# Kernel tuning notes

Measured on AMD Instinct MI355X. Metric: run time of the kernel, lower is better.

Reference implementation:

```python
import jax, jax.numpy as jnp
import numpy as np

DIM = 512
HEADS = 4
MARGIN = 1.0


def _attn_pool(x, Wq, bq, Wk, bk, Wv, bv, Wo, bo):
    # SelfAttention(video_dim, m_dim=DIM, heads=HEADS) followed by mean over time
    B, T, _ = x.shape
    hd = DIM // HEADS
    q = (x @ Wq + bq).reshape(B, T, HEADS, hd)
    k = (x @ Wk + bk).reshape(B, T, HEADS, hd)
    v = (x @ Wv + bv).reshape(B, T, HEADS, hd)
    a = jax.nn.softmax(jnp.einsum('bthd,bshd->bhts', q, k) / jnp.sqrt(jnp.float32(hd)), axis=-1)
    out = jnp.einsum('bhts,bshd->bthd', a, v).reshape(B, T, DIM) @ Wo + bo
    return out.mean(axis=1)  # [B, DIM]


def _ranking(x1, x2, gmask, margin):
    # vectorized form of the per-row torch.roll loop:
    # s[i, b] = <x1[b], x2[(b - i) mod B]>
    B = x1.shape[0]
    idx = (jnp.arange(B)[None, :] - jnp.arange(B)[:, None]) % B  # [B, B]
    s = jnp.einsum('bc,ibc->ib', x1, x2[idx])                    # [B, B]
    mask = gmask[idx] & gmask[None, :]                           # [B, B]
    # max-margin ranking loss with per-column masked mean, then mean over valid cols
    loss = jnp.maximum(0.0, margin + s[1:] - s[0:1])             # [B-1, B]
    m = mask[1:]
    cnt = m.sum(axis=0)
    col_mean = jnp.where(cnt > 0, (loss * m).sum(axis=0) / jnp.maximum(cnt, 1), 0.0)
    valid = cnt > 0
    loss_val = jnp.sum(col_mean * valid) / jnp.maximum(valid.sum(), 1)
    # ranking accuracy: idx==0 iff the true (row 0) score is max among selected
    sel_sum = jnp.sum(jnp.where(mask, s, 0.0), axis=0)
    col_valid = (sel_sum != 0) & mask.any(axis=0)
    s_masked = jnp.where(mask, s, -jnp.inf)
    top_is_first = (s[0] >= s_masked.max(axis=0)).astype(jnp.float32)
    acc = jnp.sum(jnp.where(col_valid, top_is_first, 0.0)) / jnp.maximum(col_valid.sum(), 1)
    return loss_val, jax.lax.stop_gradient(acc)


def setup_inputs() -> dict:
    key = jax.random.key(0)
    ks = iter(jax.random.split(key, 64))

    def nrm(shape, s=0.02):
        return jax.random.normal(next(ks), shape, jnp.float32) * s

    inp = {
        'o': jax.random.normal(next(ks), (128, 1024, DIM), jnp.float32),
        'rgb': jax.random.normal(next(ks), (128, 64, 2048), jnp.float32),
        'audio': jax.random.normal(next(ks), (128, 64, 128), jnp.float32),
        'group_mask': jax.random.randint(next(ks), (128,), 0, 2).astype(bool),
    }
    for name, d in (('rgb', 2048), ('audio', 128)):
        inp[f'{name}_Wq'] = nrm((d, DIM)); inp[f'{name}_bq'] = jnp.zeros((DIM,), jnp.float32)
        inp[f'{name}_Wk'] = nrm((d, DIM)); inp[f'{name}_bk'] = jnp.zeros((DIM,), jnp.float32)
        inp[f'{name}_Wv'] = nrm((d, DIM)); inp[f'{name}_bv'] = jnp.zeros((DIM,), jnp.float32)
        inp[f'{name}_Wo'] = nrm((DIM, DIM)); inp[f'{name}_bo'] = jnp.zeros((DIM,), jnp.float32)
        inp[f'{name}_W2'] = nrm((DIM, DIM)); inp[f'{name}_b2'] = jnp.zeros((DIM,), jnp.float32)
    inp['expand_W'] = nrm((DIM, 2 * DIM))
    inp['expand_b'] = jnp.zeros((2 * DIM,), jnp.float32)
    return inp


def reference(o, rgb, audio, group_mask,
              rgb_Wq, rgb_bq, rgb_Wk, rgb_bk, rgb_Wv, rgb_bv, rgb_Wo, rgb_bo, rgb_W2, rgb_b2,
              audio_Wq, audio_bq, audio_Wk, audio_bk, audio_Wv, audio_bv, audio_Wo, audio_bo,
              audio_W2, audio_b2, expand_W, expand_b):
    # per-modality encoders (CollaborativeGating multiplies are discarded in the
    # original forward, so gating is a no-op on the output -> skipped)
    f_rgb = _attn_pool(rgb, rgb_Wq, rgb_bq, rgb_Wk, rgb_bk, rgb_Wv, rgb_bv, rgb_Wo, rgb_bo) @ rgb_W2 + rgb_b2
    f_aud = _attn_pool(audio, audio_Wq, audio_bq, audio_Wk, audio_bk, audio_Wv, audio_bv, audio_Wo, audio_bo) @ audio_W2 + audio_b2
    feat = jnp.concatenate([f_rgb, f_aud], axis=-1)  # [B, 2*DIM]
    oo = o.mean(axis=-2) @ expand_W + expand_b       # [B, 2*DIM]
    oo = oo / jnp.maximum(jnp.linalg.norm(oo, axis=-1, keepdims=True), 1e-12)
    l1, a1 = _ranking(oo, feat, group_mask, MARGIN)
    l2, a2 = _ranking(feat, oo, group_mask, MARGIN)
    loss = l1 + l2
    acc = (a1 + a2) / 2.0
    return loss, acc
```

## Files before the change

kernel.cpp:

```cpp
#include <hip/hip_runtime.h>
#include <hip/hip_bf16.h>
#include <math.h>


using bf16x8 = __attribute__((ext_vector_type(8))) __bf16;
using f32x4  = __attribute__((ext_vector_type(4))) float;

enum : size_t {
  B_PART = 0,
  B_OM   = B_PART + (size_t)128*16*2*512*4,
  B_OO   = B_OM   + (size_t)128*512*4,
  B_G    = B_OO   + (size_t)128*1024*4,
  B_PP   = B_G    + (size_t)128*128*4,
  B_PO   = B_PP   + (size_t)2*128*512*4,
  B_FEAT = B_PO   + (size_t)2*128*512*4,
  B_QBF  = B_FEAT + (size_t)2*128*512*4,
  B_KBF  = B_QBF  + (size_t)2*8192*512*2,
  B_VBF  = B_KBF  + (size_t)2*8192*512*2,
  B_XR   = B_VBF  + (size_t)2*8192*512*2,
  B_XA   = B_XR   + (size_t)8192*2048*2,
  B_WT   = B_XA   + (size_t)8192*128*2,
  B_END  = B_WT   + (size_t)3*512*2048*2 + (size_t)3*512*128*2
};

__device__ __forceinline__ unsigned short f2bf(float f) {
  __hip_bfloat16 h = __float2bfloat16(f);
  return __builtin_bit_cast(unsigned short, h);
}
__device__ __forceinline__ unsigned pack2(float a, float b) {
  return (unsigned)f2bf(a) | ((unsigned)f2bf(b) << 16);
}

struct PrepArgs {
  const float* xr; unsigned short* xrb;
  const float* xa; unsigned short* xab;
  const float* w[6];
  unsigned short* wt[6];
};

__device__ __forceinline__ void castT64(const float* __restrict__ W,
                                        unsigned short* __restrict__ Wt,
                                        int K, int n0, int k0, int tid) {
  __shared__ float t[64][65];
  int c = tid & 63, r4 = tid >> 6;
#pragma unroll
  for (int i = 0; i < 16; ++i) {
    int r = r4 * 16 + i;
    t[c][r] = W[(size_t)(k0 + r) * 512 + n0 + c];
  }
  __syncthreads();
  int nr = tid >> 3, kk = (tid & 7) * 8;
#pragma unroll
  for (int p = 0; p < 2; ++p) {
    int n = nr + p * 32;
    float4 x0 = *(const float4*)&t[n][kk];
    float4 x1 = *(const float4*)&t[n][kk + 4];
    uint4 pk;
    pk.x = pack2(x0.x, x0.y); pk.y = pack2(x0.z, x0.w);
    pk.z = pack2(x1.x, x1.y); pk.w = pack2(x1.z, x1.w);
    *(uint4*)&Wt[(size_t)(n0 + n) * K + k0 + kk] = pk;
  }
}

__device__ __forceinline__ void cast8(const float* __restrict__ x,
                                      unsigned short* __restrict__ y,
                                      int i, int stride, int total) {
  for (; i < total; i += stride) {
    float4 v0 = *(const float4*)(x + (size_t)i * 8);
    float4 v1 = *(const float4*)(x + (size_t)i * 8 + 4);
    uint4 pk;
    pk.x = pack2(v0.x, v0.y); pk.y = pack2(v0.z, v0.w);
    pk.z = pack2(v1.x, v1.y); pk.w = pack2(v1.z, v1.w);
    *(uint4*)(y + (size_t)i * 8) = pk;
  }
}

__global__ __launch_bounds__(256) void prep_k(PrepArgs a) {
  int bid = blockIdx.x, tid = threadIdx.x;
  if (bid < 768) {
    int w = bid >> 8, t = bid & 255;
    castT64(a.w[w], a.wt[w], 2048, (t >> 5) * 64, (t & 31) * 64, tid);
  } else if (bid < 816) {
    int t = bid - 768; int w = t >> 4; t &= 15;
    castT64(a.w[3 + w], a.wt[3 + w], 128, (t >> 1) * 64, (t & 1) * 64, tid);
  } else if (bid < 1840) {
    cast8(a.xr, a.xrb, (bid - 816) * 256 + tid, 262144, 2097152);
  } else {
    cast8(a.xa, a.xab, (bid - 1840) * 256 + tid, 16384, 131072);
  }
}

struct QkvAll {
  const unsigned short* A[2];
  const unsigned short* Wt[6];
  const float* bias[6];
  unsigned short* out[6];
  const float* o; float* part;
};

__device__ __forceinline__ void stage16(const void* g, void* l) {
  __builtin_amdgcn_global_load_lds((const __attribute__((address_space(1))) void*)g,
                                   (__attribute__((address_space(3))) void*)l, 16, 0, 0);
}

__global__ __launch_bounds__(256) void qkv_mean_k(QkvAll args) {
  __shared__ __align__(16) char smem[32768];

  int id = blockIdx.x;
  int blk = id / 448, off = id % 448;

  if (off >= 192) {
    int mb = blk * 256 + (off - 192);
    int c = mb & 15, b = mb >> 4;
    const float* base = args.o + ((size_t)b * 1024 + (size_t)c * 64) * 512;
    int tid = threadIdx.x;
    int d4 = (tid & 127) << 2, half = tid >> 7;
    float4 s = {0.f, 0.f, 0.f, 0.f};
    for (int t = half; t < 64; t += 2) {
      float4 v = *(const float4*)(base + (size_t)t * 512 + d4);
      s.x += v.x; s.y += v.y; s.z += v.z; s.w += v.w;
    }
    *(float4*)(args.part + (((size_t)b * 16 + c) * 2 + half) * 512 + d4) = s;
    return;
  }

  int qid = blk * 192 + off;
  int mi = qid >= 768 ? 1 : 0; qid -= mi * 768;
  int by = qid & 63, bx = (qid >> 6) & 3, bz = qid >> 8;
  int K = mi ? 128 : 2048;
  int nt = K >> 5;
  const unsigned short* A = args.A[mi];
  int wi = mi * 3 + bz;
  const unsigned short* Bt = args.Wt[wi];
  const float* bias = args.bias[wi];

  int tid = threadIdx.x;
  int l = tid & 63, w = tid >> 6;
  int row0 = by * 128, col0 = bx * 128;
  int wrow = (w & 1) * 64, wcol = (w >> 1) * 64;
  int kg = l >> 4, lr = l & 15;

  float bv[4];
#pragma unroll
  for (int n = 0; n < 4; ++n) bv[n] = bias[col0 + wcol + n * 16 + lr];
  asm volatile("" :: "v"(bv[0]), "v"(bv[1]), "v"(bv[2]), "v"(bv[3]));

  auto stage_pair = [&](char* dbuf, int k0s) {
#pragma unroll
    for (int i = 0; i < 2; ++i) {
      int c = w * 128 + i * 64 + l;
      int B_ = c << 4;
      int e6 = ((B_ >> 6) ^ (B_ >> 8)) & 1;
      int E  = B_ ^ (e6 << 4) ^ (((B_ >> 7) & 1) << 5) ^ (((B_ >> 8) & 1) << 6);
      int r = E >> 6, s = ((E >> 4) & 3) << 3;
      stage16(A + (size_t)(row0 + r) * K + k0s + s, dbuf + (w * 128 + i * 64) * 16);
      stage16(Bt + (size_t)(col0 + r) * K + k0s + s, dbuf + 8192 + (w * 128 + i * 64) * 16);
    }
  };

  f32x4 acc[4][4] = {};
  int xorA = (lr & 7) << 4;

  stage_pair(smem, 0);
  int cur = 0;
  for (int t = 0; t < nt; ++t) {
    if (t + 1 < nt) {
      stage_pair(smem + ((cur ^ 1) << 14), (t + 1) << 5);
      asm volatile("s_waitcnt vmcnt(4)" ::: "memory");
    } else {
      asm volatile("s_waitcnt vmcnt(0)" ::: "memory");
    }
    __builtin_amdgcn_s_barrier();
    __builtin_amdgcn_sched_barrier(0);

    const char* Ab = smem + (cur << 14);
    const char* Bb = Ab + 8192;
    bf16x8 af[4], bfr[4];
#pragma unroll
    for (int m = 0; m < 4; ++m) {
      int ra = wrow + m * 16 + lr;
      int rb = wcol + m * 16 + lr;
      af[m]  = *(const bf16x8*)(Ab + (((ra << 6) + (kg << 4)) ^ xorA));
      bfr[m] = *(const bf16x8*)(Bb + (((rb << 6) + (kg << 4)) ^ xorA));
    }
#pragma unroll
    for (int m = 0; m < 4; ++m)
#pragma unroll
      for (int n = 0; n < 4; ++n)
        acc[m][n] = __builtin_amdgcn_mfma_f32_16x16x32_bf16(af[m], bfr[n], acc[m][n], 0, 0, 0);

    __builtin_amdgcn_sched_barrier(0);
    __builtin_amdgcn_s_barrier();
    cur ^= 1;
  }

  float* cst = (float*)(smem) + w * 1024;
  unsigned short* C = args.out[wi];
  int rr = l >> 3, q = l & 7;
#pragma unroll
  for (int m = 0; m < 4; ++m) {
#pragma unroll
    for (int n = 0; n < 4; ++n) {
      int g0 = (n * 16 + lr) >> 3, o0 = lr & 7;
#pragma unroll
      for (int j = 0; j < 4; ++j) {
        int row = kg * 4 + j;
        cst[row * 64 + (((g0 ^ (row & 7)) << 3) | o0)] = acc[m][n][j] + bv[n];
      }
    }
#pragma unroll
    for (int p = 0; p < 2; ++p) {
      int row = rr + p * 8;
      int grp = q ^ (row & 7);
      float4 x0 = *(const float4*)&cst[row * 64 + grp * 8];
      float4 x1 = *(const float4*)&cst[row * 64 + grp * 8 + 4];
      uint4 pk;
      pk.x = pack2(x0.x, x0.y); pk.y = pack2(x0.z, x0.w);
      pk.z = pack2(x1.x, x1.y); pk.w = pack2(x1.z, x1.w);
      *(uint4*)&C[(size_t)(row0 + wrow + m * 16 + row) * 512 + col0 + wcol + q * 8] = pk;
    }
  }
}

__global__ __launch_bounds__(512) void finalize_mean_k(const float* __restrict__ part,
                                                       float* __restrict__ om) {
  int b = blockIdx.x, d = threadIdx.x;
  float s = 0.f;
  for (int c = 0; c < 32; ++c) s += part[((size_t)b * 32 + c) * 512 + d];
  om[(size_t)b * 512 + d] = s * (1.f / 1024.f);
}

__global__ __launch_bounds__(256) void gemm_f32_k(
    const float* __restrict__ A, int lda,
    const float* __restrict__ W, int ldw,
    const float* __restrict__ bias,
    float* __restrict__ C, int ldc, int K) {
  __shared__ float As[16][65];
  __shared__ float Ws[16][64];
  int tid = threadIdx.x;
  int tx = tid & 15, ty = tid >> 4;
  int row0 = blockIdx.y * 64, col0 = blockIdx.x * 64;
  float acc[4][4] = {};
  int ar = tid >> 2, ac = (tid & 3) << 2;
  int wr = tid >> 4, wc = (tid & 15) << 2;
  for (int k0 = 0; k0 < K; k0 += 16) {
    float4 av = *(const float4*)(A + (size_t)(row0 + ar) * lda + k0 + ac);
    As[ac + 0][ar] = av.x; As[ac + 1][ar] = av.y;
    As[ac + 2][ar] = av.z; As[ac + 3][ar] = av.w;
    float4 wv = *(const float4*)(W + (size_t)(k0 + wr) * ldw + col0 + wc);
    *(float4*)&Ws[wr][wc] = wv;
    __syncthreads();
#pragma unroll
    for (int k = 0; k < 16; ++k) {
      float a0 = As[k][(ty << 2) + 0], a1 = As[k][(ty << 2) + 1];
      float a2 = As[k][(ty << 2) + 2], a3 = As[k][(ty << 2) + 3];
      float4 w = *(const float4*)&Ws[k][tx << 2];
      acc[0][0] += a0 * w.x; acc[0][1] += a0 * w.y; acc[0][2] += a0 * w.z; acc[0][3] += a0 * w.w;
      acc[1][0] += a1 * w.x; acc[1][1] += a1 * w.y; acc[1][2] += a1 * w.z; acc[1][3] += a1 * w.w;
      acc[2][0] += a2 * w.x; acc[2][1] += a2 * w.y; acc[2][2] += a2 * w.z; acc[2][3] += a2 * w.w;
      acc[3][0] += a3 * w.x; acc[3][1] += a3 * w.y; acc[3][2] += a3 * w.z; acc[3][3] += a3 * w.w;
    }
    __syncthreads();
  }
  float4 bv = *(const float4*)(bias + col0 + (tx << 2));
#pragma unroll
  for (int i = 0; i < 4; ++i) {
    float4 ov;
    ov.x = acc[i][0] + bv.x; ov.y = acc[i][1] + bv.y;
    ov.z = acc[i][2] + bv.z; ov.w = acc[i][3] + bv.w;
    *(float4*)(C + (size_t)(row0 + (ty << 2) + i) * ldc + col0 + (tx << 2)) = ov;
  }
}

__global__ __launch_bounds__(256) void gemm_f32_2w_k(
    const float* __restrict__ A,
    const float* __restrict__ W0, const float* __restrict__ W1,
    const float* __restrict__ b0, const float* __restrict__ b1,
    float* __restrict__ C) {
  const float* W = (blockIdx.y >= 2) ? W1 : W0;
  const float* bias = (blockIdx.y >= 2) ? b1 : b0;
  __shared__ float As[16][65];
  __shared__ float Ws[16][64];
  int tid = threadIdx.x;
  int tx = tid & 15, ty = tid >> 4;
  int row0 = blockIdx.y * 64, col0 = blockIdx.x * 64;
  float acc[4][4] = {};
  int ar = tid >> 2, ac = (tid & 3) << 2;
  int wr = tid >> 4, wc = (tid & 15) << 2;
  for (int k0 = 0; k0 < 512; k0 += 16) {
    float4 av = *(const float4*)(A + (size_t)(row0 + ar) * 512 + k0 + ac);
    As[ac + 0][ar] = av.x; As[ac + 1][ar] = av.y;
    As[ac + 2][ar] = av.z; As[ac + 3][ar] = av.w;
    float4 wv = *(const float4*)(W + (size_t)(k0 + wr) * 512 + col0 + wc);
    *(float4*)&Ws[wr][wc] = wv;
    __syncthreads();
#pragma unroll
    for (int k = 0; k < 16; ++k) {
      float a0 = As[k][(ty << 2) + 0], a1 = As[k][(ty << 2) + 1];
      float a2 = As[k][(ty << 2) + 2], a3 = As[k][(ty << 2) + 3];
      float4 w = *(const float4*)&Ws[k][tx << 2];
      acc[0][0] += a0 * w.x; acc[0][1] += a0 * w.y; acc[0][2] += a0 * w.z; acc[0][3] += a0 * w.w;
      acc[1][0] += a1 * w.x; acc[1][1] += a1 * w.y; acc[1][2] += a1 * w.z; acc[1][3] += a1 * w.w;
      acc[2][0] += a2 * w.x; acc[2][1] += a2 * w.y; acc[2][2] += a2 * w.z; acc[2][3] += a2 * w.w;
      acc[3][0] += a3 * w.x; acc[3][1] += a3 * w.y; acc[3][2] += a3 * w.z; acc[3][3] += a3 * w.w;
    }
    __syncthreads();
  }
  float4 bv = *(const float4*)(bias + col0 + (tx << 2));
#pragma unroll
  for (int i = 0; i < 4; ++i) {
    float4 ov;
    ov.x = acc[i][0] + bv.x; ov.y = acc[i][1] + bv.y;
    ov.z = acc[i][2] + bv.z; ov.w = acc[i][3] + bv.w;
    *(float4*)(C + (size_t)(row0 + (ty << 2) + i) * 512 + col0 + (tx << 2)) = ov;
  }
}

__global__ __launch_bounds__(256) void attn_pool_k(
    const unsigned short* __restrict__ qbf,
    const unsigned short* __restrict__ kbf,
    const unsigned short* __restrict__ vbf,
    float* __restrict__ pooled) {
  __shared__ float wlds[4][64];
  int b = blockIdx.x, m = blockIdx.y;
  int tid = threadIdx.x;
  int w = tid >> 6, l = tid & 63, lr = l & 15, g = l >> 4;
  size_t base = ((size_t)m * 8192 + (size_t)b * 64) * 512 + w * 128;

  bf16x8 qf[4][4];
#pragma unroll
  for (int tb = 0; tb < 4; ++tb)
#pragma unroll
    for (int ks = 0; ks < 4; ++ks)
      qf[tb][ks] = *(const bf16x8*)(qbf + base + (size_t)(tb * 16 + lr) * 512 + ks * 32 + g * 8);

  f32x4 acc[4][4] = {};
#pragma unroll
  for (int sb = 0; sb < 4; ++sb) {
    bf16x8 kf[4];
#pragma unroll
    for (int ks = 0; ks < 4; ++ks)
      kf[ks] = *(const bf16x8*)(kbf + base + (size_t)(sb * 16 + lr) * 512 + ks * 32 + g * 8);
#pragma unroll
    for (int tb = 0; tb < 4; ++tb)
#pragma unroll
      for (int ks = 0; ks < 4; ++ks)
        acc[sb][tb] = __builtin_amdgcn_mfma_f32_16x16x32_bf16(kf[ks], qf[tb][ks], acc[sb][tb], 0, 0, 0);
  }

  const float scale = 0.08838834764831845f;
  float mx[4] = {-INFINITY, -INFINITY, -INFINITY, -INFINITY};
#pragma unroll
  for (int sb = 0; sb < 4; ++sb)
#pragma unroll
    for (int tb = 0; tb < 4; ++tb)
#pragma unroll
      for (int j = 0; j < 4; ++j) {
        acc[sb][tb][j] *= scale;
        mx[tb] = fmaxf(mx[tb], acc[sb][tb][j]);
      }
#pragma unroll
  for (int tb = 0; tb < 4; ++tb) {
    mx[tb] = fmaxf(mx[tb], __shfl_xor(mx[tb], 16));
    mx[tb] = fmaxf(mx[tb], __shfl_xor(mx[tb], 32));
  }
  float sm[4] = {0.f, 0.f, 0.f, 0.f};
#pragma unroll
  for (int sb = 0; sb < 4; ++sb)
#pragma unroll
    for (int tb = 0; tb < 4; ++tb)
#pragma unroll
      for (int j = 0; j < 4; ++j) {
        float e = expf(acc[sb][tb][j] - mx[tb]);
        acc[sb][tb][j] = e;
        sm[tb] += e;
      }
  float inv[4];
#pragma unroll
  for (int tb = 0; tb < 4; ++tb) {
    sm[tb] += __shfl_xor(sm[tb], 16);
    sm[tb] += __shfl_xor(sm[tb], 32);
    inv[tb] = 1.f / sm[tb];
  }
#pragma unroll
  for (int sb = 0; sb < 4; ++sb)
#pragma unroll
    for (int j = 0; j < 4; ++j) {
      float cs = acc[sb][0][j] * inv[0] + acc[sb][1][j] * inv[1]
               + acc[sb][2][j] * inv[2] + acc[sb][3][j] * inv[3];
      cs += __shfl_xor(cs, 1);
      cs += __shfl_xor(cs, 2);
      cs += __shfl_xor(cs, 4);
      cs += __shfl_xor(cs, 8);
      if (lr == 0) wlds[w][sb * 16 + g * 4 + j] = cs * (1.f / 64.f);
    }
  __syncthreads();

  int h = tid >> 6, c2 = (tid & 63) << 1;
  size_t vbase = ((size_t)m * 8192 + (size_t)b * 64) * 512 + h * 128 + c2;
  float s0 = 0.f, s1 = 0.f;
#pragma unroll 8
  for (int s = 0; s < 64; ++s) {
    unsigned u = *(const unsigned*)(vbf + vbase + (size_t)s * 512);
    float vlo = __builtin_bit_cast(float, u << 16);
    float vhi = __builtin_bit_cast(float, u & 0xffff0000u);
    float wv = wlds[h][s];
    s0 += wv * vlo; s1 += wv * vhi;
  }
  float2 o2 = {s0, s1};
  *(float2*)(pooled + ((size_t)m * 128 + b) * 512 + h * 128 + c2) = o2;
}

__global__ __launch_bounds__(256) void ntg_k(const float* __restrict__ oo,
                                             const float* __restrict__ feat,
                                             float* __restrict__ G) {
  __shared__ float As[16][33], Bs[16][33];
  __shared__ float inv32[32];
  int tid = threadIdx.x;
  int row0 = blockIdx.y * 32, col0 = blockIdx.x * 32;
  int ar = tid >> 3, aq = tid & 7;
  int ty = tid >> 4, tx = tid & 15;
  float acc[2][2] = {};
  float ssq = 0.f;
  for (int k0 = 0; k0 < 1024; k0 += 16) {
    float2 av = *(const float2*)(oo + (size_t)(row0 + ar) * 1024 + k0 + aq * 2);
    As[aq * 2 + 0][ar] = av.x;
    As[aq * 2 + 1][ar] = av.y;
    ssq += av.x * av.x + av.y * av.y;
    int kk = k0 + aq * 2;
    float2 bv = *(const float2*)(feat + (size_t)((kk >> 9) * 128 + col0 + ar) * 512 + (kk & 511));
    Bs[aq * 2 + 0][ar] = bv.x;
    Bs[aq * 2 + 1][ar] = bv.y;
    __syncthreads();
#pragma unroll
    for (int k = 0; k < 16; ++k) {
      float a0 = As[k][ty * 2], a1 = As[k][ty * 2 + 1];
      float b0 = Bs[k][tx * 2], b1 = Bs[k][tx * 2 + 1];
      acc[0][0] += a0 * b0; acc[0][1] += a0 * b1;
      acc[1][0] += a1 * b0; acc[1][1] += a1 * b1;
    }
    __syncthreads();
  }
  ssq += __shfl_xor(ssq, 1);
  ssq += __shfl_xor(ssq, 2);
  ssq += __shfl_xor(ssq, 4);
  if (aq == 0) inv32[ar] = 1.f / fmaxf(sqrtf(ssq), 1e-12f);
  __syncthreads();
#pragma unroll
  for (int i = 0; i < 2; ++i)
#pragma unroll
    for (int j = 0; j < 2; ++j)
      G[(size_t)(row0 + ty * 2 + i) * 128 + col0 + tx * 2 + j] = acc[i][j] * inv32[ty * 2 + i];
}

__global__ __launch_bounds__(128) void final_k(const float* __restrict__ G,
                                               const int* __restrict__ gmask,
                                               float* __restrict__ out) {
  __shared__ float cm[2][128], vd[2][128], tp[2][128], cv[2][128];
  __shared__ int gm[128];
  int b = threadIdx.x;
  gm[b] = gmask[b];
  __syncthreads();
  for (int r = 0; r < 2; ++r) {
    bool gb = gm[b] != 0;
    float s0 = G[b * 128 + b];
    int cnt = 0;
    float lsum = 0.f, selsum = 0.f, smax = -INFINITY;
    bool anym = false;
    for (int i = 0; i < 128; ++i) {
      int j = (b - i + 128) & 127;
      bool mk = gb && (gm[j] != 0);
      float sv = (r == 0) ? G[b * 128 + j] : G[j * 128 + b];
      if (mk) {
        selsum += sv; anym = true;
        smax = fmaxf(smax, sv);
        if (i >= 1) { cnt++; lsum += fmaxf(0.f, 1.f + sv - s0); }
      }
    }
    cm[r][b] = (cnt > 0) ? (lsum / (float)cnt) : 0.f;
    vd[r][b] = (cnt > 0) ? 1.f : 0.f;
    bool colvalid = (selsum != 0.f) && anym;
    tp[r][b] = (colvalid && (s0 >= smax)) ? 1.f : 0.f;
    cv[r][b] = colvalid ? 1.f : 0.f;
  }
  __syncthreads();
  if (b == 0) {
    float loss = 0.f, acc = 0.f;
    for (int r = 0; r < 2; ++r) {
      float scm = 0, svd = 0, stp = 0, scv = 0;
      for (int i = 0; i < 128; ++i) { scm += cm[r][i]; svd += vd[r][i]; stp += tp[r][i]; scv += cv[r][i]; }
      loss += scm / fmaxf(svd, 1.f);
      acc += stp / fmaxf(scv, 1.f);
    }
    out[0] = loss;
    out[1] = acc * 0.5f;
  }
}

extern "C" void kernel_launch(void* const* d_in, const int* in_sizes, int n_in,
                              void* d_out, int out_size, void* d_ws, size_t ws_size,
                              hipStream_t stream) {
  const float* o     = (const float*)d_in[0];
  const float* rgb   = (const float*)d_in[1];
  const float* audio = (const float*)d_in[2];
  const int* gmask   = (const int*)d_in[3];
  const float* W[2][10];
  for (int m = 0; m < 2; ++m)
    for (int w = 0; w < 10; ++w) W[m][w] = (const float*)d_in[4 + m * 10 + w];
  const float* expand_W = (const float*)d_in[24];
  const float* expand_b = (const float*)d_in[25];

  char* ws = (char*)d_ws;
  float* part = (float*)(ws + B_PART);
  float* om   = (float*)(ws + B_OM);
  float* oo   = (float*)(ws + B_OO);
  float* G    = (float*)(ws + B_G);
  float* pp2  = (float*)(ws + B_PP);
  float* po2  = (float*)(ws + B_PO);
  float* feat2= (float*)(ws + B_FEAT);
  unsigned short* qbf = (unsigned short*)(ws + B_QBF);
  unsigned short* kbf = (unsigned short*)(ws + B_KBF);
  unsigned short* vbf = (unsigned short*)(ws + B_VBF);
  unsigned short* xrb = (unsigned short*)(ws + B_XR);
  unsigned short* xab = (unsigned short*)(ws + B_XA);
  unsigned short* wt  = (unsigned short*)(ws + B_WT);
  unsigned short* wtp[6];
  wtp[0] = wt;
  wtp[1] = wtp[0] + (size_t)512 * 2048;
  wtp[2] = wtp[1] + (size_t)512 * 2048;
  wtp[3] = wtp[2] + (size_t)512 * 2048;
  wtp[4] = wtp[3] + (size_t)512 * 128;
  wtp[5] = wtp[4] + (size_t)512 * 128;

  PrepArgs pa;
  pa.xr = rgb;   pa.xrb = xrb;
  pa.xa = audio; pa.xab = xab;
  pa.w[0] = W[0][0]; pa.w[1] = W[0][2]; pa.w[2] = W[0][4];
  pa.w[3] = W[1][0]; pa.w[4] = W[1][2]; pa.w[5] = W[1][4];
  for (int i = 0; i < 6; ++i) pa.wt[i] = wtp[i];
  prep_k<<<1904, 256, 0, stream>>>(pa);

  QkvAll qa;
  qa.A[0] = xrb; qa.A[1] = xab;
  for (int i = 0; i < 6; ++i) qa.Wt[i] = wtp[i];
  qa.bias[0] = W[0][1]; qa.bias[1] = W[0][3]; qa.bias[2] = W[0][5];
  qa.bias[3] = W[1][1]; qa.bias[4] = W[1][3]; qa.bias[5] = W[1][5];
  qa.out[0] = qbf;                       qa.out[1] = kbf;                       qa.out[2] = vbf;
  qa.out[3] = qbf + (size_t)8192 * 512;  qa.out[4] = kbf + (size_t)8192 * 512;  qa.out[5] = vbf + (size_t)8192 * 512;
  qa.o = o; qa.part = part;
  qkv_mean_k<<<3584, 256, 0, stream>>>(qa);

  finalize_mean_k<<<128, 512, 0, stream>>>(part, om);
  gemm_f32_k<<<dim3(16, 2), 256, 0, stream>>>(om, 512, expand_W, 1024, expand_b, oo, 1024, 512);

  attn_pool_k<<<dim3(128, 2), 256, 0, stream>>>(qbf, kbf, vbf, pp2);

  gemm_f32_2w_k<<<dim3(8, 4), 256, 0, stream>>>(pp2, W[0][6], W[1][6], W[0][7], W[1][7], po2);
  gemm_f32_2w_k<<<dim3(8, 4), 256, 0, stream>>>(po2, W[0][8], W[1][8], W[0][9], W[1][9], feat2);

  ntg_k<<<dim3(4, 4), 256, 0, stream>>>(oo, feat2, G);
  final_k<<<1, 128, 0, stream>>>(G, gmask, (float*)d_out);
}
```

Measured before the change: 382.6 us.

## Widen QKV GEMM tiles to 128x256 and drop LDS swizzle

Each QKV projection GEMM block now computes a 128x256 output tile instead of 128x128, with every wave owning 64x128 and reusing one A fragment across eight B fragments. This halves the number of GEMM blocks and cuts repeated loads of A. LDS per block grows to 48KB, which lowers occupancy. The XOR swizzle on LDS staging and reads is removed in favour of plain row-major layout, so bank conflicts on the 64-byte rows may return. The epilogue now transposes through a padded stride-17 buffer.

```diff
diff --git a/kernel.cpp b/kernel.cpp
--- a/kernel.cpp
+++ b/kernel.cpp
@@ -104,13 +104,13 @@
 }
 
 __global__ __launch_bounds__(256) void qkv_mean_k(QkvAll args) {
-  __shared__ __align__(16) char smem[32768];
+  __shared__ __align__(16) char smem[49152];
 
   int id = blockIdx.x;
-  int blk = id / 448, off = id % 448;
-
-  if (off >= 192) {
-    int mb = blk * 256 + (off - 192);
+  int blk = id / 352, off = id % 352;
+
+  if (off >= 96) {
+    int mb = blk * 256 + (off - 96);
     int c = mb & 15, b = mb >> 4;
     const float* base = args.o + ((size_t)b * 1024 + (size_t)c * 64) * 512;
     int tid = threadIdx.x;
@@ -124,9 +124,9 @@
     return;
   }
 
-  int qid = blk * 192 + off;
-  int mi = qid >= 768 ? 1 : 0; qid -= mi * 768;
-  int by = qid & 63, bx = (qid >> 6) & 3, bz = qid >> 8;
+  int qid = blk * 96 + off;
+  int mi = qid >= 384 ? 1 : 0; qid -= mi * 384;
+  int by = qid & 63, bx = (qid >> 6) & 1, bz = qid >> 7;
   int K = mi ? 128 : 2048;
   int nt = K >> 5;
   const unsigned short* A = args.A[mi];
@@ -135,89 +135,85 @@
   const float* bias = args.bias[wi];
 
   int tid = threadIdx.x;
-  int l = tid & 63, w = tid >> 6;
-  int row0 = by * 128, col0 = bx * 128;
-  int wrow = (w & 1) * 64, wcol = (w >> 1) * 64;
+  int l = tid & 63, wid = tid >> 6;
+  int wr = wid >> 1, wc = wid & 1;
+  int row0 = by * 128, col0 = bx * 256;
   int kg = l >> 4, lr = l & 15;
 
-  float bv[4];
-#pragma unroll
-  for (int n = 0; n < 4; ++n) bv[n] = bias[col0 + wcol + n * 16 + lr];
-  asm volatile("" :: "v"(bv[0]), "v"(bv[1]), "v"(bv[2]), "v"(bv[3]));
-
-  auto stage_pair = [&](char* dbuf, int k0s) {
+  float bv[8];
+#pragma unroll
+  for (int n = 0; n < 8; ++n) bv[n] = bias[col0 + wc * 128 + n * 16 + lr];
+  asm volatile("" :: "v"(bv[0]), "v"(bv[1]), "v"(bv[2]), "v"(bv[3]),
+                     "v"(bv[4]), "v"(bv[5]), "v"(bv[6]), "v"(bv[7]));
+
+  auto stage_step = [&](char* dbuf, int k0s) {
 #pragma unroll
     for (int i = 0; i < 2; ++i) {
-      int c = w * 128 + i * 64 + l;
-      int B_ = c << 4;
-      int e6 = ((B_ >> 6) ^ (B_ >> 8)) & 1;
-      int E  = B_ ^ (e6 << 4) ^ (((B_ >> 7) & 1) << 5) ^ (((B_ >> 8) & 1) << 6);
-      int r = E >> 6, s = ((E >> 4) & 3) << 3;
-      stage16(A + (size_t)(row0 + r) * K + k0s + s, dbuf + (w * 128 + i * 64) * 16);
-      stage16(Bt + (size_t)(col0 + r) * K + k0s + s, dbuf + 8192 + (w * 128 + i * 64) * 16);
+      int c = i * 256 + tid;
+      int r = c >> 2, s = (c & 3) << 3;
+      stage16(A + (size_t)(row0 + r) * K + k0s + s, dbuf + c * 16);
+    }
+#pragma unroll
+    for (int i = 0; i < 4; ++i) {
+      int c = i * 256 + tid;
+      int r = c >> 2, s = (c & 3) << 3;
+      stage16(Bt + (size_t)(col0 + r) * K + k0s + s, dbuf + 8192 + c * 16);
     }
   };
 
-  f32x4 acc[4][4] = {};
-  int xorA = (lr & 7) << 4;
-
-  stage_pair(smem, 0);
+  f32x4 acc[4][8] = {};
+
+  stage_step(smem, 0);
   int cur = 0;
   for (int t = 0; t < nt; ++t) {
     if (t + 1 < nt) {
-      stage_pair(smem + ((cur ^ 1) << 14), (t + 1) << 5);
-      asm volatile("s_waitcnt vmcnt(4)" ::: "memory");
+      stage_step(smem + (cur ^ 1) * 24576, (t + 1) << 5);
+      asm volatile("s_waitcnt vmcnt(6)" ::: "memory");
     } else {
       asm volatile("s_waitcnt vmcnt(0)" ::: "memory");
     }
     __builtin_amdgcn_s_barrier();
     __builtin_amdgcn_sched_barrier(0);
 
-    const char* Ab = smem + (cur << 14);
+    const char* Ab = smem + cur * 24576;
     const char* Bb = Ab + 8192;
-    bf16x8 af[4], bfr[4];
+    bf16x8 bfr[8];
+#pragma unroll
+    for (int n = 0; n < 8; ++n)
+      bfr[n] = *(const bf16x8*)(Bb + (wc * 128 + n * 16 + lr) * 64 + kg * 16);
 #pragma unroll
     for (int m = 0; m < 4; ++m) {
-      int ra = wrow + m * 16 + lr;
-      int rb = wcol + m * 16 + lr;
-      af[m]  = *(const bf16x8*)(Ab + (((ra << 6) + (kg << 4)) ^ xorA));
-      bfr[m] = *(const bf16x8*)(Bb + (((rb << 6) + (kg << 4)) ^ xorA));
-    }
-#pragma unroll
-    for (int m = 0; m < 4; ++m)
-#pragma unroll
-      for (int n = 0; n < 4; ++n)
-        acc[m][n] = __builtin_amdgcn_mfma_f32_16x16x32_bf16(af[m], bfr[n], acc[m][n], 0, 0, 0);
+      bf16x8 af = *(const bf16x8*)(Ab + (wr * 64 + m * 16 + lr) * 64 + kg * 16);
+#pragma unroll
+      for (int n = 0; n < 8; ++n)
+        acc[m][n] = __builtin_amdgcn_mfma_f32_16x16x32_bf16(af, bfr[n], acc[m][n], 0, 0, 0);
+    }
 
     __builtin_amdgcn_sched_barrier(0);
     __builtin_amdgcn_s_barrier();
     cur ^= 1;
   }
 
-  float* cst = (float*)(smem) + w * 1024;
+  float* cst = (float*)smem + wid * 2176;
   unsigned short* C = args.out[wi];
-  int rr = l >> 3, q = l & 7;
+  int q = l & 15, rb = l >> 4;
 #pragma unroll
   for (int m = 0; m < 4; ++m) {
 #pragma unroll
-    for (int n = 0; n < 4; ++n) {
-      int g0 = (n * 16 + lr) >> 3, o0 = lr & 7;
-#pragma unroll
-      for (int j = 0; j < 4; ++j) {
-        int row = kg * 4 + j;
-        cst[row * 64 + (((g0 ^ (row & 7)) << 3) | o0)] = acc[m][n][j] + bv[n];
-      }
-    }
-#pragma unroll
-    for (int p = 0; p < 2; ++p) {
-      int row = rr + p * 8;
-      int grp = q ^ (row & 7);
-      float4 x0 = *(const float4*)&cst[row * 64 + grp * 8];
-      float4 x1 = *(const float4*)&cst[row * 64 + grp * 8 + 4];
+    for (int n = 0; n < 8; ++n)
+#pragma unroll
+      for (int j = 0; j < 4; ++j)
+        cst[(n * 16 + lr) * 17 + kg * 4 + j] = acc[m][n][j] + bv[n];
+#pragma unroll
+    for (int p = 0; p < 4; ++p) {
+      int row = p * 4 + rb;
+      float v[8];
+#pragma unroll
+      for (int i = 0; i < 8; ++i) v[i] = cst[(q * 8 + i) * 17 + row];
       uint4 pk;
-      pk.x = pack2(x0.x, x0.y); pk.y = pack2(x0.z, x0.w);
-      pk.z = pack2(x1.x, x1.y); pk.w = pack2(x1.z, x1.w);
-      *(uint4*)&C[(size_t)(row0 + wrow + m * 16 + row) * 512 + col0 + wcol + q * 8] = pk;
+      pk.x = pack2(v[0], v[1]); pk.y = pack2(v[2], v[3]);
+      pk.z = pack2(v[4], v[5]); pk.w = pack2(v[6], v[7]);
+      *(uint4*)&C[(size_t)(row0 + wr * 64 + m * 16 + row) * 512 + col0 + wc * 128 + q * 8] = pk;
     }
   }
 }
@@ -548,7 +544,7 @@
   qa.out[0] = qbf;                       qa.out[1] = kbf;                       qa.out[2] = vbf;
   qa.out[3] = qbf + (size_t)8192 * 512;  qa.out[4] = kbf + (size_t)8192 * 512;  qa.out[5] = vbf + (size_t)8192 * 512;
   qa.o = o; qa.part = part;
-  qkv_mean_k<<<3584, 256, 0, stream>>>(qa);
+  qkv_mean_k<<<2816, 256, 0, stream>>>(qa);
 
   finalize_mean_k<<<128, 512, 0, stream>>>(part, om);
   gemm_f32_k<<<dim3(16, 2), 256, 0, stream>>>(om, 512, expand_W, 1024, expand_b, oo, 1024, 512);
```

After: 457.4 us. 19.5% more time.

## Fuse small tail kernels via last-block atomic counters and merged launches

Applied to the files above, without the earlier changes.

Removes the separate mean-finalize kernel by having the last of each batch's 16 partial-sum blocks reduce the partials, using an atomic counter. The expand GEMM and attention-pool kernels are merged into a single launch, and the final ranking-loss kernel is folded into the NTG GEMM through a last-block-done counter. The intent is to cut launch overhead and idle gaps between tiny dependent kernels. In exchange it adds threadfences, atomics and counters reset in prep_k, and the final reduction runs serially in a single block.

```diff
diff --git a/kernel.cpp b/kernel.cpp
--- a/kernel.cpp
+++ b/kernel.cpp
@@ -8,7 +8,7 @@
 
 enum : size_t {
   B_PART = 0,
-  B_OM   = B_PART + (size_t)128*16*2*512*4,
+  B_OM   = B_PART + (size_t)128*32*512*4,
   B_OO   = B_OM   + (size_t)128*512*4,
   B_G    = B_OO   + (size_t)128*1024*4,
   B_PP   = B_G    + (size_t)128*128*4,
@@ -20,7 +20,8 @@
   B_XR   = B_VBF  + (size_t)2*8192*512*2,
   B_XA   = B_XR   + (size_t)8192*2048*2,
   B_WT   = B_XA   + (size_t)8192*128*2,
-  B_END  = B_WT   + (size_t)3*512*2048*2 + (size_t)3*512*128*2
+  B_CNT  = B_WT   + (size_t)3*512*2048*2 + (size_t)3*512*128*2,
+  B_END  = B_CNT + 1024
 };
 
 __device__ __forceinline__ unsigned short f2bf(float f) {
@@ -36,6 +37,7 @@
   const float* xa; unsigned short* xab;
   const float* w[6];
   unsigned short* wt[6];
+  unsigned* cnt;
 };
 
 __device__ __forceinline__ void castT64(const float* __restrict__ W,
@@ -77,6 +79,8 @@
 
 __global__ __launch_bounds__(256) void prep_k(PrepArgs a) {
   int bid = blockIdx.x, tid = threadIdx.x;
+  if (bid == 0 && tid < 129)
+    __hip_atomic_store(a.cnt + tid, 0u, __ATOMIC_RELAXED, __HIP_MEMORY_SCOPE_AGENT);
   if (bid < 768) {
     int w = bid >> 8, t = bid & 255;
     castT64(a.w[w], a.wt[w], 2048, (t >> 5) * 64, (t & 31) * 64, tid);
@@ -95,7 +99,8 @@
   const unsigned short* Wt[6];
   const float* bias[6];
   unsigned short* out[6];
-  const float* o; float* part;
+  const float* o; float* part; float* om;
+  unsigned* cnt;
 };
 
 __device__ __forceinline__ void stage16(const void* g, void* l) {
@@ -120,7 +125,28 @@
       float4 v = *(const float4*)(base + (size_t)t * 512 + d4);
       s.x += v.x; s.y += v.y; s.z += v.z; s.w += v.w;
     }
-    *(float4*)(args.part + (((size_t)b * 16 + c) * 2 + half) * 512 + d4) = s;
+    *(float4*)(args.part + ((size_t)b * 32 + c * 2 + half) * 512 + d4) = s;
+
+    __threadfence();
+    __syncthreads();
+    __shared__ int win;
+    if (tid == 0) {
+      unsigned prev = __hip_atomic_fetch_add(args.cnt + b, 1u,
+                        __ATOMIC_ACQ_REL, __HIP_MEMORY_SCOPE_AGENT);
+      win = (prev == 15u);
+    }
+    __syncthreads();
+    if (win) {
+      __threadfence();
+#pragma unroll
+      for (int p = 0; p < 2; ++p) {
+        int d = tid + p * 256;
+        float s2 = 0.f;
+        for (int r = 0; r < 32; ++r)
+          s2 += args.part[((size_t)b * 32 + r) * 512 + d];
+        args.om[(size_t)b * 512 + d] = s2 * (1.f / 1024.f);
+      }
+    }
     return;
   }
 
@@ -222,24 +248,16 @@
   }
 }
 
-__global__ __launch_bounds__(512) void finalize_mean_k(const float* __restrict__ part,
-                                                       float* __restrict__ om) {
-  int b = blockIdx.x, d = threadIdx.x;
-  float s = 0.f;
-  for (int c = 0; c < 32; ++c) s += part[((size_t)b * 32 + c) * 512 + d];
-  om[(size_t)b * 512 + d] = s * (1.f / 1024.f);
-}
-
-__global__ __launch_bounds__(256) void gemm_f32_k(
-    const float* __restrict__ A, int lda,
-    const float* __restrict__ W, int ldw,
-    const float* __restrict__ bias,
-    float* __restrict__ C, int ldc, int K) {
+__device__ void gemm_dev(const float* __restrict__ A, int lda,
+                         const float* __restrict__ W, int ldw,
+                         const float* __restrict__ bias,
+                         float* __restrict__ C, int ldc, int K,
+                         int bx, int by) {
   __shared__ float As[16][65];
   __shared__ float Ws[16][64];
   int tid = threadIdx.x;
   int tx = tid & 15, ty = tid >> 4;
-  int row0 = blockIdx.y * 64, col0 = blockIdx.x * 64;
+  int row0 = by * 64, col0 = bx * 64;
   float acc[4][4] = {};
   int ar = tid >> 2, ac = (tid & 3) << 2;
   int wr = tid >> 4, wc = (tid & 15) << 2;
@@ -272,57 +290,11 @@
   }
 }
 
-__global__ __launch_bounds__(256) void gemm_f32_2w_k(
-    const float* __restrict__ A,
-    const float* __restrict__ W0, const float* __restrict__ W1,
-    const float* __restrict__ b0, const float* __restrict__ b1,
-    float* __restrict__ C) {
-  const float* W = (blockIdx.y >= 2) ? W1 : W0;
-  const float* bias = (blockIdx.y >= 2) ? b1 : b0;
-  __shared__ float As[16][65];
-  __shared__ float Ws[16][64];
-  int tid = threadIdx.x;
-  int tx = tid & 15, ty = tid >> 4;
-  int row0 = blockIdx.y * 64, col0 = blockIdx.x * 64;
-  float acc[4][4] = {};
-  int ar = tid >> 2, ac = (tid & 3) << 2;
-  int wr = tid >> 4, wc = (tid & 15) << 2;
-  for (int k0 = 0; k0 < 512; k0 += 16) {
-    float4 av = *(const float4*)(A + (size_t)(row0 + ar) * 512 + k0 + ac);
-    As[ac + 0][ar] = av.x; As[ac + 1][ar] = av.y;
-    As[ac + 2][ar] = av.z; As[ac + 3][ar] = av.w;
-    float4 wv = *(const float4*)(W + (size_t)(k0 + wr) * 512 + col0 + wc);
-    *(float4*)&Ws[wr][wc] = wv;
-    __syncthreads();
-#pragma unroll
-    for (int k = 0; k < 16; ++k) {
-      float a0 = As[k][(ty << 2) + 0], a1 = As[k][(ty << 2) + 1];
-      float a2 = As[k][(ty << 2) + 2], a3 = As[k][(ty << 2) + 3];
-      float4 w = *(const float4*)&Ws[k][tx << 2];
-      acc[0][0] += a0 * w.x; acc[0][1] += a0 * w.y; acc[0][2] += a0 * w.z; acc[0][3] += a0 * w.w;
-      acc[1][0] += a1 * w.x; acc[1][1] += a1 * w.y; acc[1][2] += a1 * w.z; acc[1][3] += a1 * w.w;
-      acc[2][0] += a2 * w.x; acc[2][1] += a2 * w.y; acc[2][2] += a2 * w.z; acc[2][3] += a2 * w.w;
-      acc[3][0] += a3 * w.x; acc[3][1] += a3 * w.y; acc[3][2] += a3 * w.z; acc[3][3] += a3 * w.w;
-    }
-    __syncthreads();
-  }
-  float4 bv = *(const float4*)(bias + col0 + (tx << 2));
-#pragma unroll
-  for (int i = 0; i < 4; ++i) {
-    float4 ov;
-    ov.x = acc[i][0] + bv.x; ov.y = acc[i][1] + bv.y;
-    ov.z = acc[i][2] + bv.z; ov.w = acc[i][3] + bv.w;
-    *(float4*)(C + (size_t)(row0 + (ty << 2) + i) * 512 + col0 + (tx << 2)) = ov;
-  }
-}
-
-__global__ __launch_bounds__(256) void attn_pool_k(
-    const unsigned short* __restrict__ qbf,
-    const unsigned short* __restrict__ kbf,
-    const unsigned short* __restrict__ vbf,
-    float* __restrict__ pooled) {
+__device__ void attn_dev(const unsigned short* __restrict__ qbf,
+                         const unsigned short* __restrict__ kbf,
+                         const unsigned short* __restrict__ vbf,
+                         float* __restrict__ pooled, int b, int m) {
   __shared__ float wlds[4][64];
-  int b = blockIdx.x, m = blockIdx.y;
   int tid = threadIdx.x;
   int w = tid >> 6, l = tid & 63, lr = l & 15, g = l >> 4;
   size_t base = ((size_t)m * 8192 + (size_t)b * 64) * 512 + w * 128;
@@ -411,77 +383,70 @@
   *(float2*)(pooled + ((size_t)m * 128 + b) * 512 + h * 128 + c2) = o2;
 }
 
-__global__ __launch_bounds__(256) void ntg_k(const float* __restrict__ oo,
-                                             const float* __restrict__ feat,
-                                             float* __restrict__ G) {
-  __shared__ float As[16][33], Bs[16][33];
-  __shared__ float inv32[32];
-  int tid = threadIdx.x;
-  int row0 = blockIdx.y * 32, col0 = blockIdx.x * 32;
-  int ar = tid >> 3, aq = tid & 7;
-  int ty = tid >> 4, tx = tid & 15;
-  float acc[2][2] = {};
-  float ssq = 0.f;
-  for (int k0 = 0; k0 < 1024; k0 += 16) {
-    float2 av = *(const float2*)(oo + (size_t)(row0 + ar) * 1024 + k0 + aq * 2);
-    As[aq * 2 + 0][ar] = av.x;
-    As[aq * 2 + 1][ar] = av.y;
-    ssq += av.x * av.x + av.y * av.y;
-    int kk = k0 + aq * 2;
-    float2 bv = *(const float2*)(feat + (size_t)((kk >> 9) * 128 + col0 + ar) * 512 + (kk & 511));
-    Bs[aq * 2 + 0][ar] = bv.x;
-    Bs[aq * 2 + 1][ar] = bv.y;
-    __syncthreads();
-#pragma unroll
-    for (int k = 0; k < 16; ++k) {
-      float a0 = As[k][ty * 2], a1 = As[k][ty * 2 + 1];
-      float b0 = Bs[k][tx * 2], b1 = Bs[k][tx * 2 + 1];
-      acc[0][0] += a0 * b0; acc[0][1] += a0 * b1;
-      acc[1][0] += a1 * b0; acc[1][1] += a1 * b1;
-    }
-    __syncthreads();
-  }
-  ssq += __shfl_xor(ssq, 1);
-  ssq += __shfl_xor(ssq, 2);
-  ssq += __shfl_xor(ssq, 4);
-  if (aq == 0) inv32[ar] = 1.f / fmaxf(sqrtf(ssq), 1e-12f);
-  __syncthreads();
-#pragma unroll
-  for (int i = 0; i < 2; ++i)
-#pragma unroll
-    for (int j = 0; j < 2; ++j)
-      G[(size_t)(row0 + ty * 2 + i) * 128 + col0 + tx * 2 + j] = acc[i][j] * inv32[ty * 2 + i];
-}
-
-__global__ __launch_bounds__(128) void final_k(const float* __restrict__ G,
-                                               const int* __restrict__ gmask,
-                                               float* __restrict__ out) {
+struct MidArgs {
+  const float* om; const float* expand_W; const float* expand_b; float* oo;
+  const unsigned short* qbf; const unsigned short* kbf; const unsigned short* vbf;
+  float* pp;
+};
+
+__global__ __launch_bounds__(256) void mid_k(MidArgs a) {
+  int blk = blockIdx.x;
+  if (blk < 32) {
+    gemm_dev(a.om, 512, a.expand_W, 1024, a.expand_b, a.oo, 1024, 512,
+             blk & 15, blk >> 4);
+  } else {
+    int t = blk - 32;
+    attn_dev(a.qbf, a.kbf, a.vbf, a.pp, t & 127, t >> 7);
+  }
+}
+
+__global__ __launch_bounds__(256) void gemm_f32_2w_k(
+    const float* __restrict__ A,
+    const float* __restrict__ W0, const float* __restrict__ W1,
+    const float* __restrict__ b0, const float* __restrict__ b1,
+    float* __restrict__ C) {
+  const float* W = (blockIdx.y >= 2) ? W1 : W0;
+  const float* bias = (blockIdx.y >= 2) ? b1 : b0;
+  gemm_dev(A, 512, W, 512, bias, C, 512, 512, blockIdx.x, blockIdx.y);
+}
+
+struct NtgfArgs {
+  const float* oo; const float* feat; float* G;
+  const int* gmask; float* out;
+  unsigned* cnt;
+};
+
+__device__ void final_dev(const float* __restrict__ G,
+                          const int* __restrict__ gmask,
+                          float* __restrict__ out) {
   __shared__ float cm[2][128], vd[2][128], tp[2][128], cv[2][128];
   __shared__ int gm[128];
   int b = threadIdx.x;
-  gm[b] = gmask[b];
+  if (b < 128) gm[b] = gmask[b];
   __syncthreads();
-  for (int r = 0; r < 2; ++r) {
-    bool gb = gm[b] != 0;
-    float s0 = G[b * 128 + b];
-    int cnt = 0;
-    float lsum = 0.f, selsum = 0.f, smax = -INFINITY;
-    bool anym = false;
-    for (int i = 0; i < 128; ++i) {
-      int j = (b - i + 128) & 127;
-      bool mk = gb && (gm[j] != 0);
-      float sv = (r == 0) ? G[b * 128 + j] : G[j * 128 + b];
-      if (mk) {
-        selsum += sv; anym = true;
-        smax = fmaxf(smax, sv);
-        if (i >= 1) { cnt++; lsum += fmaxf(0.f, 1.f + sv - s0); }
+  if (b < 128) {
+    for (int r = 0; r < 2; ++r) {
+      bool gb = gm[b] != 0;
+      float s0 = G[b * 128 + b];
+      int cnt = 0;
+      float lsum = 0.f, selsum = 0.f, smax = -INFINITY;
+      bool anym = false;
+      for (int i = 0; i < 128; ++i) {
+        int j = (b - i + 128) & 127;
+        bool mk = gb && (gm[j] != 0);
+        float sv = (r == 0) ? G[b * 128 + j] : G[j * 128 + b];
+        if (mk) {
+          selsum += sv; anym = true;
+          smax = fmaxf(smax, sv);
+          if (i >= 1) { cnt++; lsum += fmaxf(0.f, 1.f + sv - s0); }
+        }
       }
-    }
-    cm[r][b] = (cnt > 0) ? (lsum / (float)cnt) : 0.f;
-    vd[r][b] = (cnt > 0) ? 1.f : 0.f;
-    bool colvalid = (selsum != 0.f) && anym;
-    tp[r][b] = (colvalid && (s0 >= smax)) ? 1.f : 0.f;
-    cv[r][b] = colvalid ? 1.f : 0.f;
+      cm[r][b] = (cnt > 0) ? (lsum / (float)cnt) : 0.f;
+      vd[r][b] = (cnt > 0) ? 1.f : 0.f;
+      bool colvalid = (selsum != 0.f) && anym;
+      tp[r][b] = (colvalid && (s0 >= smax)) ? 1.f : 0.f;
+      cv[r][b] = colvalid ? 1.f : 0.f;
+    }
   }
   __syncthreads();
   if (b == 0) {
@@ -494,6 +459,63 @@
     }
     out[0] = loss;
     out[1] = acc * 0.5f;
+  }
+}
+
+__global__ __launch_bounds__(256) void ntgf_k(NtgfArgs a) {
+  {
+    __shared__ float As[16][33], Bs[16][33];
+    __shared__ float inv32[32];
+    int tid = threadIdx.x;
+    int bx = blockIdx.x & 3, by = blockIdx.x >> 2;
+    int row0 = by * 32, col0 = bx * 32;
+    int ar = tid >> 3, aq = tid & 7;
+    int ty = tid >> 4, tx = tid & 15;
+    float acc[2][2] = {};
+    float ssq = 0.f;
+    for (int k0 = 0; k0 < 1024; k0 += 16) {
+      float2 av = *(const float2*)(a.oo + (size_t)(row0 + ar) * 1024 + k0 + aq * 2);
+      As[aq * 2 + 0][ar] = av.x;
+      As[aq * 2 + 1][ar] = av.y;
+      ssq += av.x * av.x + av.y * av.y;
+      int kk = k0 + aq * 2;
+      float2 bv = *(const float2*)(a.feat + (size_t)((kk >> 9) * 128 + col0 + ar) * 512 + (kk & 511));
+      Bs[aq * 2 + 0][ar] = bv.x;
+      Bs[aq * 2 + 1][ar] = bv.y;
+      __syncthreads();
+#pragma unroll
+      for (int k = 0; k < 16; ++k) {
+        float a0 = As[k][ty * 2], a1 = As[k][ty * 2 + 1];
+        float b0 = Bs[k][tx * 2], b1 = Bs[k][tx * 2 + 1];
+        acc[0][0] += a0 * b0; acc[0][1] += a0 * b1;
+        acc[1][0] += a1 * b0; acc[1][1] += a1 * b1;
+      }
+      __syncthreads();
+    }
+    ssq += __shfl_xor(ssq, 1);
+    ssq += __shfl_xor(ssq, 2);
+    ssq += __shfl_xor(ssq, 4);
+    if (aq == 0) inv32[ar] = 1.f / fmaxf(sqrtf(ssq), 1e-12f);
+    __syncthreads();
+#pragma unroll
+    for (int i = 0; i < 2; ++i)
+#pragma unroll
+      for (int j = 0; j < 2; ++j)
+        a.G[(size_t)(row0 + ty * 2 + i) * 128 + col0 + tx * 2 + j] = acc[i][j] * inv32[ty * 2 + i];
+  }
+
+  __threadfence();
+  __syncthreads();
+  __shared__ int win;
+  if (threadIdx.x == 0) {
+    unsigned prev = __hip_atomic_fetch_add(a.cnt + 128, 1u,
+                      __ATOMIC_ACQ_REL, __HIP_MEMORY_SCOPE_AGENT);
+    win = (prev == 15u);
+  }
+  __syncthreads();
+  if (win) {
+    __threadfence();
+    final_dev(a.G, a.gmask, a.out);
   }
 }
 
@@ -524,6 +546,7 @@
   unsigned short* xrb = (unsigned short*)(ws + B_XR);
   unsigned short* xab = (unsigned short*)(ws + B_XA);
   unsigned short* wt  = (unsigned short*)(ws + B_WT);
+  unsigned* cnt = (unsigned*)(ws + B_CNT);
   unsigned short* wtp[6];
   wtp[0] = wt;
   wtp[1] = wtp[0] + (size_t)512 * 2048;
@@ -538,6 +561,7 @@
   pa.w[0] = W[0][0]; pa.w[1] = W[0][2]; pa.w[2] = W[0][4];
   pa.w[3] = W[1][0]; pa.w[4] = W[1][2]; pa.w[5] = W[1][4];
   for (int i = 0; i < 6; ++i) pa.wt[i] = wtp[i];
+  pa.cnt = cnt;
   prep_k<<<1904, 256, 0, stream>>>(pa);
 
   QkvAll qa;
@@ -547,17 +571,19 @@
   qa.bias[3] = W[1][1]; qa.bias[4] = W[1][3]; qa.bias[5] = W[1][5];
   qa.out[0] = qbf;                       qa.out[1] = kbf;                       qa.out[2] = vbf;
   qa.out[3] = qbf + (size_t)8192 * 512;  qa.out[4] = kbf + (size_t)8192 * 512;  qa.out[5] = vbf + (size_t)8192 * 512;
-  qa.o = o; qa.part = part;
+  qa.o = o; qa.part = part; qa.om = om; qa.cnt = cnt;
   qkv_mean_k<<<3584, 256, 0, stream>>>(qa);
 
-  finalize_mean_k<<<128, 512, 0, stream>>>(part, om);
-  gemm_f32_k<<<dim3(16, 2), 256, 0, stream>>>(om, 512, expand_W, 1024, expand_b, oo, 1024, 512);
-
-  attn_pool_k<<<dim3(128, 2), 256, 0, stream>>>(qbf, kbf, vbf, pp2);
+  MidArgs ma;
+  ma.om = om; ma.expand_W = expand_W; ma.expand_b = expand_b; ma.oo = oo;
+  ma.qbf = qbf; ma.kbf = kbf; ma.vbf = vbf; ma.pp = pp2;
+  mid_k<<<288, 256, 0, stream>>>(ma);
 
   gemm_f32_2w_k<<<dim3(8, 4), 256, 0, stream>>>(pp2, W[0][6], W[1][6], W[0][7], W[1][7], po2);
   gemm_f32_2w_k<<<dim3(8, 4), 256, 0, stream>>>(po2, W[0][8], W[1][8], W[0][9], W[1][9], feat2);
 
-  ntg_k<<<dim3(4, 4), 256, 0, stream>>>(oo, feat2, G);
-  final_k<<<1, 128, 0, stream>>>(G, gmask, (float*)d_out);
-}
+  NtgfArgs na;
+  na.oo = oo; na.feat = feat2; na.G = G; na.gmask = gmask;
+  na.out = (float*)d_out; na.cnt = cnt;
+  ntgf_k<<<16, 256, 0, stream>>>(na);
+}
```

Result: slower. 950.8 us (+148.5%).
